# Kernel optimization log

Measured on AMD Instinct MI355X. Metric: run time of the kernel, lower is better.

The kernel has to match this reference:

```python
import jax, jax.numpy as jnp
import numpy as np

EMBED_DIM = 1024
ZDIM = 128
STD = 0.02


def setup_inputs() -> dict:
    key = jax.random.key(0)
    ks = jax.random.split(key, 12)
    T, S, B, E, Z = 2048, 2048, 4, EMBED_DIM, ZDIM
    return {
        "query": jax.random.normal(ks[0], (T, B, E), jnp.float32),
        "key": jax.random.normal(ks[1], (S, B, E), jnp.float32),
        "Wq": jax.random.normal(ks[2], (2 * E + Z, E), jnp.float32) * STD,
        "bq": jnp.zeros((2 * E + Z,), jnp.float32),
        "Wk": jax.random.normal(ks[3], (Z, E), jnp.float32) * STD,
        "bk": jnp.zeros((Z,), jnp.float32),
        "Wv": jax.random.normal(ks[4], (E, E), jnp.float32) * STD,
        "bv": jnp.zeros((E,), jnp.float32),
        "Wh": jax.random.normal(ks[5], (E, E), jnp.float32) * STD,
        "bh": jnp.zeros((E,), jnp.float32),
        "gamma": jax.random.normal(ks[6], (2, Z), jnp.float32) * STD,
        "beta": jnp.zeros((2, Z), jnp.float32),
    }


def reference(query, key, Wq, bq, Wk, bk, Wv, bv, Wh, bh, gamma, beta):
    E, Z = EMBED_DIM, ZDIM
    scaling = Z ** (-0.5)
    # base: [T, B, 2E+Z]
    base = jnp.einsum('tbe,fe->tbf', query, Wq) + bq
    u = jax.nn.sigmoid(base[..., :E])                      # [T,B,E] output gate
    rq = jax.nn.silu(base[..., E:])                        # [T,B,E+Z]
    r = rq[..., :E]                                        # [T,B,E]
    q = rq[..., E:] * gamma[0] + beta[0]                   # [T,B,Z]
    k = jax.nn.silu(jnp.einsum('sbe,ze->sbz', key, Wk) + bk) * gamma[1] + beta[1]  # [S,B,Z]
    v = jax.nn.silu(jnp.einsum('sbe,fe->sbf', key, Wv) + bv)                       # [S,B,E]
    # softmax attention over context dim
    qk = jnp.einsum('tbz,sbz->bts', q * scaling, k)        # [B,T,S]
    attn = jax.nn.softmax(qk, axis=-1)
    h = jnp.einsum('bts,sbf->tbf', attn, v)                # [T,B,E]
    h = jnp.tanh(jnp.einsum('tbe,fe->tbf', h * r, Wh) + bh)
    out = query + u * (h - query)                          # addcmul
    return out
```

## Files before the change

kernel.cpp:

```cpp
#include <hip/hip_runtime.h>
#include <cstdint>
#include <cstddef>

using short8  = __attribute__((ext_vector_type(8))) short;
using floatx4 = __attribute__((ext_vector_type(4))) float;

#define DEV __device__ __forceinline__

DEV float u2f(unsigned short u){
  union { unsigned int i; float f; } c; c.i = ((unsigned int)u) << 16; return c.f;
}
DEV unsigned short f2u(float f){
  union { float f; unsigned int i; } c; c.f = f;
  unsigned int i = c.i;
  i += 0x7fffu + ((i >> 16) & 1u);
  return (unsigned short)(i >> 16);
}
DEV float sigmoidf_(float x){ return 1.0f / (1.0f + __expf(-x)); }
DEV float siluf_(float x){ return x / (1.0f + __expf(-x)); }

#define ASYNC_LD16(g, l) __builtin_amdgcn_global_load_lds( \
    (const __attribute__((address_space(1))) unsigned int*)(g), \
    (__attribute__((address_space(3))) unsigned int*)(l), 16, 0, 0)

#define MFMA_BF16 __builtin_amdgcn_mfma_f32_16x16x32_bf16

#define SBAR() asm volatile("s_barrier" ::: "memory")
#define LGKM0() asm volatile("s_waitcnt lgkmcnt(0)" ::: "memory")

constexpr float SCALING = 0.088388347648318447f;

__global__ __launch_bounds__(256) void cast_all(
    const float* __restrict__ q, const float* __restrict__ k,
    const float* __restrict__ Wq, const float* __restrict__ Wk,
    const float* __restrict__ Wv, const float* __restrict__ Wh,
    unsigned short* __restrict__ qo, unsigned short* __restrict__ ko,
    unsigned short* __restrict__ oq, unsigned short* __restrict__ ok,
    unsigned short* __restrict__ ov, unsigned short* __restrict__ oh)
{
  const int bid = blockIdx.x;
  const int e = threadIdx.x * 4;
  const float* src; unsigned short* dst;
  if (bid < 8192) {
    src = q + (long long)bid * 1024;
    dst = qo + (long long)bid * 1024;
  } else if (bid < 16384) {
    const int m = bid - 8192;
    const int s = m >> 2, b = m & 3;
    src = k + (long long)m * 1024;
    dst = ko + ((long long)b * 2048 + s) * 1024;
  } else if (bid < 18560) { src = Wq + (long long)(bid-16384) * 1024; dst = oq + (long long)(bid-16384) * 1024; }
  else if (bid < 18688)   { src = Wk + (long long)(bid-18560) * 1024; dst = ok + (long long)(bid-18560) * 1024; }
  else if (bid < 19712)   { src = Wv + (long long)(bid-18688) * 1024; dst = ov + (long long)(bid-18688) * 1024; }
  else                    { src = Wh + (long long)(bid-19712) * 1024; dst = oh + (long long)(bid-19712) * 1024; }
  const float4 v = *(const float4*)(src + e);
  ushort4 o; o.x=f2u(v.x); o.y=f2u(v.y); o.z=f2u(v.z); o.w=f2u(v.w);
  *(ushort4*)(dst + e) = o;
}

__global__ __launch_bounds__(512, 2)
void mega(const unsigned short* __restrict__ qbf,
          const unsigned short* __restrict__ Wqb,
          const unsigned short* __restrict__ kbr,
          const unsigned short* __restrict__ Wvb,
          const unsigned short* __restrict__ Wkb,
          const float* __restrict__ bq, const float* __restrict__ bk,
          const float* __restrict__ bv,
          const float* __restrict__ gamma, const float* __restrict__ beta,
          float* __restrict__ ub_f,
          unsigned short* __restrict__ rbf,
          unsigned short* __restrict__ vT,
          unsigned short* __restrict__ qpj,
          unsigned short* __restrict__ kpj)
{
  __shared__ __align__(16) unsigned short Ls[65536];

  const int bid = blockIdx.x;
  const int tid = threadIdx.x;
  const int lane = tid & 63;
  const int wv   = tid >> 6;
  const int lr   = lane & 15;
  const int lq   = lane >> 4;
  const int r7   = lr & 7;

  const floatx4 zero = {0.f, 0.f, 0.f, 0.f};

  if (bid < 256) {
    const int bm = bid & 31, bn = bid >> 5;
    const int row0 = bm * 256;
    const int col0 = bn * 256;
    const int lda = 1024, ldb = 1024;
    const int wr = (wv >> 2) * 128;
    const int wc = (wv & 3) * 64;

    const int rr0 = tid >> 3;
    const int swz = ((tid & 7) ^ (rr0 & 7)) * 8;
    const unsigned short* gA0 = qbf + (long long)(row0 + rr0) * lda + swz;
    const unsigned short* gB0 = Wqb + (long long)(col0 + rr0) * ldb + swz;
    const long long sA64 = 64LL * lda, sB64 = 64LL * ldb;
    unsigned short* lA0 = &Ls[0]     + tid * 8;
    unsigned short* lB0 = &Ls[16384] + tid * 8;

    floatx4 acc[8][4];
    #pragma unroll
    for (int i = 0; i < 8; i++)
      #pragma unroll
      for (int j = 0; j < 4; j++) acc[i][j] = zero;

    const int NT = 16;

    #pragma unroll
    for (int i = 0; i < 4; i++) ASYNC_LD16(gA0 + i * sA64,      lA0 + i * 4096);
    #pragma unroll
    for (int i = 0; i < 4; i++) ASYNC_LD16(gB0 + i * sB64,      lB0 + i * 4096);
    #pragma unroll
    for (int i = 0; i < 4; i++) ASYNC_LD16(gA0 + i * sA64 + 64, lA0 + i * 4096 + 32768);
    #pragma unroll
    for (int i = 0; i < 4; i++) ASYNC_LD16(gB0 + i * sB64 + 64, lB0 + i * 4096 + 32768);
    asm volatile("s_waitcnt vmcnt(8)" ::: "memory");
    SBAR();

    for (int t = 0; t < NT; ++t) {
      const int cb = (t & 1) << 15;
      const unsigned short* Ab = &Ls[cb];
      const unsigned short* Bb = &Ls[cb + 16384];
      const bool st = (t + 2) < NT;
      const int kt2 = (t + 2) << 6;

      short8 afA[4][2], afB[4][2], bf01[2][2], bf23[2][2];

      #pragma unroll
      for (int mi = 0; mi < 4; mi++)
        #pragma unroll
        for (int kk = 0; kk < 2; kk++)
          afA[mi][kk] = *(const short8*)(Ab + (wr + mi*16 + lr) * 64 + (((kk<<2) + lq) ^ r7) * 8);
      #pragma unroll
      for (int ni = 0; ni < 2; ni++)
        #pragma unroll
        for (int kk = 0; kk < 2; kk++)
          bf01[ni][kk] = *(const short8*)(Bb + (wc + ni*16 + lr) * 64 + (((kk<<2) + lq) ^ r7) * 8);
      #pragma unroll
      for (int ni = 0; ni < 2; ni++)
        #pragma unroll
        for (int kk = 0; kk < 2; kk++)
          bf23[ni][kk] = *(const short8*)(Bb + (wc + (ni+2)*16 + lr) * 64 + (((kk<<2) + lq) ^ r7) * 8);
      __builtin_amdgcn_s_setprio(1);
      #pragma unroll
      for (int mi = 0; mi < 4; mi++)
        #pragma unroll
        for (int ni = 0; ni < 2; ni++)
          #pragma unroll
          for (int kk = 0; kk < 2; kk++)
            acc[mi][ni] = MFMA_BF16(afA[mi][kk], bf01[ni][kk], acc[mi][ni], 0, 0, 0);
      #pragma unroll
      for (int mi = 0; mi < 4; mi++)
        #pragma unroll
        for (int ni = 0; ni < 2; ni++)
          #pragma unroll
          for (int kk = 0; kk < 2; kk++)
            acc[mi][ni+2] = MFMA_BF16(afA[mi][kk], bf23[ni][kk], acc[mi][ni+2], 0, 0, 0);
      __builtin_amdgcn_s_setprio(0);
      LGKM0();
      SBAR();

      #pragma unroll
      for (int mi = 0; mi < 4; mi++)
        #pragma unroll
        for (int kk = 0; kk < 2; kk++)
          afB[mi][kk] = *(const short8*)(Ab + (wr + (mi+4)*16 + lr) * 64 + (((kk<<2) + lq) ^ r7) * 8);
      if (st) {
        #pragma unroll
        for (int i = 0; i < 4; i++) ASYNC_LD16(gB0 + i * sB64 + kt2, lB0 + i * 4096 + cb);
      }
      __builtin_amdgcn_s_setprio(1);
      #pragma unroll
      for (int mi = 0; mi < 4; mi++)
        #pragma unroll
        for (int ni = 0; ni < 2; ni++)
          #pragma unroll
          for (int kk = 0; kk < 2; kk++)
            acc[mi+4][ni] = MFMA_BF16(afB[mi][kk], bf01[ni][kk], acc[mi+4][ni], 0, 0, 0);
      __builtin_amdgcn_s_setprio(0);
      LGKM0();
      SBAR();

      if (st) {
        #pragma unroll
        for (int i = 0; i < 4; i++) ASYNC_LD16(gA0 + i * sA64 + kt2, lA0 + i * 4096 + cb);
      }
      __builtin_amdgcn_s_setprio(1);
      #pragma unroll
      for (int mi = 0; mi < 4; mi++)
        #pragma unroll
        for (int ni = 0; ni < 2; ni++)
          #pragma unroll
          for (int kk = 0; kk < 2; kk++)
            acc[mi+4][ni+2] = MFMA_BF16(afB[mi][kk], bf23[ni][kk], acc[mi+4][ni+2], 0, 0, 0);
      __builtin_amdgcn_s_setprio(0);
      if (st) { asm volatile("s_waitcnt vmcnt(8)" ::: "memory"); }
      else    { asm volatile("s_waitcnt vmcnt(0)" ::: "memory"); }
      SBAR();
    }

    #pragma unroll
    for (int mi = 0; mi < 8; mi++)
      #pragma unroll
      for (int ni = 0; ni < 4; ni++)
        #pragma unroll
        for (int r = 0; r < 4; r++) {
          const int gm = row0 + wr + mi * 16 + lq * 4 + r;
          const int gn = col0 + wc + ni * 16 + lr;
          float v = acc[mi][ni][r] + bq[gn];
          if (gn < 1024) {
            ((unsigned short*)ub_f)[(long long)gm * 1024 + gn] = f2u(sigmoidf_(v));
          } else {
            rbf[(long long)gm * 1024 + (gn - 1024)] = f2u(siluf_(v));
          }
        }
  } else {
    const unsigned short* Ag; const unsigned short* Bg;
    int row0, col0, zproj = -1;
    if (bid < 512) {
      const int idx = bid - 256;
      row0 = (idx & 3) * 256;
      col0 = (idx >> 2) * 128;
      Ag = Wvb; Bg = kbr;
    } else {
      const int idx = bid - 512;
      zproj = idx >> 5;
      row0 = (idx & 31) * 256;
      col0 = 0;
      Ag = zproj ? kbr : qbf;
      Bg = zproj ? Wkb : (Wqb + 2048LL * 1024);
    }
    const int lda = 1024, ldb = 1024;
    const int wr = (wv & 3) * 64;
    const int wc = (wv >> 2) * 64;

    const int rr0 = tid >> 3;
    const int swz = ((tid & 7) ^ (rr0 & 7)) * 8;
    const unsigned short* gA0 = Ag + (long long)(row0 + rr0) * lda + swz;
    const unsigned short* gB0 = Bg + (long long)(col0 + rr0) * ldb + swz;
    const long long sA64 = 64LL * lda, sB64 = 64LL * ldb;
    unsigned short* lA0 = &Ls[0]     + tid * 8;
    unsigned short* lB0 = &Ls[16384] + tid * 8;

    floatx4 acc[4][4];
    #pragma unroll
    for (int i = 0; i < 4; i++)
      #pragma unroll
      for (int j = 0; j < 4; j++) acc[i][j] = zero;

    const int NT = 16;

    #pragma unroll
    for (int i = 0; i < 4; i++) ASYNC_LD16(gA0 + i * sA64,      lA0 + i * 4096);
    #pragma unroll
    for (int i = 0; i < 2; i++) ASYNC_LD16(gB0 + i * sB64,      lB0 + i * 4096);
    #pragma unroll
    for (int i = 0; i < 4; i++) ASYNC_LD16(gA0 + i * sA64 + 64, lA0 + i * 4096 + 24576);
    #pragma unroll
    for (int i = 0; i < 2; i++) ASYNC_LD16(gB0 + i * sB64 + 64, lB0 + i * 4096 + 24576);
    asm volatile("s_waitcnt vmcnt(6)" ::: "memory");
    SBAR();

    for (int t = 0; t < NT; ++t) {
      const int cb = (t & 1) * 24576;
      const unsigned short* Ab = &Ls[cb];
      const unsigned short* Bb = &Ls[cb + 16384];
      const bool st = (t + 2) < NT;
      const int kt2 = (t + 2) << 6;

      short8 afA[4][2], bfv[4][2];

      #pragma unroll
      for (int mi = 0; mi < 4; mi++)
        #pragma unroll
        for (int kk = 0; kk < 2; kk++)
          afA[mi][kk] = *(const short8*)(Ab + (wr + mi*16 + lr) * 64 + (((kk<<2) + lq) ^ r7) * 8);
      #pragma unroll
      for (int ni = 0; ni < 4; ni++)
        #pragma unroll
        for (int kk = 0; kk < 2; kk++)
          bfv[ni][kk] = *(const short8*)(Bb + (wc + ni*16 + lr) * 64 + (((kk<<2) + lq) ^ r7) * 8);
      LGKM0();
      __builtin_amdgcn_sched_barrier(0);
      __builtin_amdgcn_s_setprio(1);
      #pragma unroll
      for (int mi = 0; mi < 4; mi++)
        #pragma unroll
        for (int ni = 0; ni < 2; ni++)
          #pragma unroll
          for (int kk = 0; kk < 2; kk++)
            acc[mi][ni] = MFMA_BF16(afA[mi][kk], bfv[ni][kk], acc[mi][ni], 0, 0, 0);
      __builtin_amdgcn_s_setprio(0);
      SBAR();

      if (st) {
        #pragma unroll
        for (int i = 0; i < 4; i++) ASYNC_LD16(gA0 + i * sA64 + kt2, lA0 + i * 4096 + cb);
        #pragma unroll
        for (int i = 0; i < 2; i++) ASYNC_LD16(gB0 + i * sB64 + kt2, lB0 + i * 4096 + cb);
      }
      __builtin_amdgcn_s_setprio(1);
      #pragma unroll
      for (int mi = 0; mi < 4; mi++)
        #pragma unroll
        for (int ni = 0; ni < 2; ni++)
          #pragma unroll
          for (int kk = 0; kk < 2; kk++)
            acc[mi][ni+2] = MFMA_BF16(afA[mi][kk], bfv[ni+2][kk], acc[mi][ni+2], 0, 0, 0);
      __builtin_amdgcn_s_setprio(0);
      if (st) { asm volatile("s_waitcnt vmcnt(6)" ::: "memory"); }
      else    { asm volatile("s_waitcnt vmcnt(0)" ::: "memory"); }
      SBAR();
    }

    if (zproj < 0) {
      #pragma unroll
      for (int mi = 0; mi < 4; mi++)
        #pragma unroll
        for (int ni = 0; ni < 4; ni++)
          #pragma unroll
          for (int r = 0; r < 4; r++) {
            const int gm = row0 + wr + mi * 16 + lq * 4 + r;
            const int gn = col0 + wc + ni * 16 + lr;
            const float v = acc[mi][ni][r] + bv[gm];
            const int b = gn >> 11, s = gn & 2047;
            vT[((long long)b * 1024 + gm) * 2048 + s] = f2u(siluf_(v));
          }
    } else {
      const float* bias = zproj ? bk : (bq + 2048);
      const float* gam  = zproj ? (gamma + 128) : gamma;
      const float* bet  = zproj ? (beta + 128)  : beta;
      unsigned short* ob = zproj ? kpj : qpj;
      #pragma unroll
      for (int mi = 0; mi < 4; mi++)
        #pragma unroll
        for (int ni = 0; ni < 4; ni++)
          #pragma unroll
          for (int r = 0; r < 4; r++) {
            const int gm = row0 + wr + mi * 16 + lq * 4 + r;
            const int gn = wc + ni * 16 + lr;
            const float v = acc[mi][ni][r] + bias[gn];
            ob[(long long)gm * 128 + gn] = f2u(siluf_(v) * gam[gn] + bet[gn]);
          }
    }
  }
}

__global__ __launch_bounds__(512, 2)
void gemm_g5(const unsigned short* __restrict__ A, int lda,
             const unsigned short* __restrict__ Bm, int ldb,
             int K,
             const float* __restrict__ bias,
             float* __restrict__ f0,
             const unsigned short* __restrict__ rmul,
             const float* __restrict__ qin)
{
  __shared__ __align__(16) unsigned short Ls[49152];

  const int tid = threadIdx.x;
  const int bm = blockIdx.x, bn = blockIdx.y;
  const int row0 = bm * 256;
  const int col0 = bn * 128;

  const int lane = tid & 63;
  const int wv   = tid >> 6;
  const int wr   = (wv & 3) * 64;
  const int wc   = (wv >> 2) * 64;
  const int lr   = lane & 15;
  const int lq   = lane >> 4;
  const int r7   = lr & 7;

  const int rr0 = tid >> 3;
  const int swz = ((tid & 7) ^ (rr0 & 7)) * 8;
  const unsigned short* gA0 = A  + (long long)(row0 + rr0) * lda + swz;
  const unsigned short* gB0 = Bm + (long long)(col0 + rr0) * ldb + swz;
  const long long sA64 = 64LL * lda, sB64 = 64LL * ldb;
  unsigned short* lA0 = &Ls[0]     + tid * 8;
  unsigned short* lB0 = &Ls[16384] + tid * 8;

  floatx4 acc[4][4];
  const floatx4 zero = {0.f, 0.f, 0.f, 0.f};
  #pragma unroll
  for (int i = 0; i < 4; i++)
    #pragma unroll
    for (int j = 0; j < 4; j++) acc[i][j] = zero;

  const int NT = K >> 6;

  #pragma unroll
  for (int i = 0; i < 4; i++) ASYNC_LD16(gA0 + i * sA64,      lA0 + i * 4096);
  #pragma unroll
  for (int i = 0; i < 2; i++) ASYNC_LD16(gB0 + i * sB64,      lB0 + i * 4096);
  #pragma unroll
  for (int i = 0; i < 4; i++) ASYNC_LD16(gA0 + i * sA64 + 64, lA0 + i * 4096 + 24576);
  #pragma unroll
  for (int i = 0; i < 2; i++) ASYNC_LD16(gB0 + i * sB64 + 64, lB0 + i * 4096 + 24576);
  asm volatile("s_waitcnt vmcnt(6)" ::: "memory");
  SBAR();

  for (int t = 0; t < NT; ++t) {
    const int cb = (t & 1) * 24576;
    const unsigned short* Ab = &Ls[cb];
    const unsigned short* Bb = &Ls[cb + 16384];
    const bool st = (t + 2) < NT;
    const int kt2 = (t + 2) << 6;

    short8 afA[4][2], bfv[4][2];

    #pragma unroll
    for (int mi = 0; mi < 4; mi++)
      #pragma unroll
      for (int kk = 0; kk < 2; kk++)
        afA[mi][kk] = *(const short8*)(Ab + (wr + mi*16 + lr) * 64 + (((kk<<2) + lq) ^ r7) * 8);
    #pragma unroll
    for (int ni = 0; ni < 4; ni++)
      #pragma unroll
      for (int kk = 0; kk < 2; kk++)
        bfv[ni][kk] = *(const short8*)(Bb + (wc + ni*16 + lr) * 64 + (((kk<<2) + lq) ^ r7) * 8);
    LGKM0();
    __builtin_amdgcn_sched_barrier(0);
    __builtin_amdgcn_s_setprio(1);
    #pragma unroll
    for (int mi = 0; mi < 4; mi++)
      #pragma unroll
      for (int ni = 0; ni < 2; ni++)
        #pragma unroll
        for (int kk = 0; kk < 2; kk++)
          acc[mi][ni] = MFMA_BF16(afA[mi][kk], bfv[ni][kk], acc[mi][ni], 0, 0, 0);
    __builtin_amdgcn_s_setprio(0);
    SBAR();

    if (st) {
      #pragma unroll
      for (int i = 0; i < 4; i++) ASYNC_LD16(gA0 + i * sA64 + kt2, lA0 + i * 4096 + cb);
      #pragma unroll
      for (int i = 0; i < 2; i++) ASYNC_LD16(gB0 + i * sB64 + kt2, lB0 + i * 4096 + cb);
    }
    __builtin_amdgcn_s_setprio(1);
    #pragma unroll
    for (int mi = 0; mi < 4; mi++)
      #pragma unroll
      for (int ni = 0; ni < 2; ni++)
        #pragma unroll
        for (int kk = 0; kk < 2; kk++)
          acc[mi][ni+2] = MFMA_BF16(afA[mi][kk], bfv[ni+2][kk], acc[mi][ni+2], 0, 0, 0);
    __builtin_amdgcn_s_setprio(0);
    if (st) { asm volatile("s_waitcnt vmcnt(6)" ::: "memory"); }
    else    { asm volatile("s_waitcnt vmcnt(0)" ::: "memory"); }
    SBAR();
  }

  #pragma unroll
  for (int mi = 0; mi < 4; mi++)
    #pragma unroll
    for (int ni = 0; ni < 4; ni++)
      #pragma unroll
      for (int r = 0; r < 4; r++) {
        const int gm = row0 + wr + mi * 16 + lq * 4 + r;
        const int gn = col0 + wc + ni * 16 + lr;
        const long long idx = (long long)gm * 1024 + gn;
        const float tv = tanhf(acc[mi][ni][r] + bias[gn]);
        const float qv = qin[idx];
        f0[idx] = qv + u2f(rmul[idx]) * (tv - qv);
      }
}

__global__ __launch_bounds__(512, 2)
void attn_fused(const unsigned short* __restrict__ qpj,
                const unsigned short* __restrict__ kpj,
                const unsigned short* __restrict__ vT,
                const unsigned short* __restrict__ rbf,
                unsigned short* __restrict__ hrb)
{
  __shared__ __align__(16) unsigned short Vs[32768];
  __shared__ __align__(16) unsigned short Ks[2][8192];
  __shared__ __align__(16) unsigned short Ps[4096];
  __shared__ float rsl[64];

  const int tid = threadIdx.x;
  const int eh = blockIdx.x, ty = blockIdx.y, bz = blockIdx.z;
  const int t0 = ty * 64;

  const int lane = tid & 63;
  const int wv   = tid >> 6;
  const int lr   = lane & 15;
  const int lq   = lane >> 4;
  const int mi_s = wv & 3;
  const int niA  = (wv >> 2) * 2;

  const unsigned short* kb_g = kpj + (long long)bz * 2048 * 128;
  const unsigned short* vb_g = vT  + (long long)bz * 1024 * 2048;

  short8 afq[4];
  {
    const unsigned short* qrow = qpj + (long long)bz * 128
                               + (long long)(t0 + mi_s * 16 + lr) * 512;
    #pragma unroll
    for (int kd = 0; kd < 4; kd++)
      afq[kd] = *(const short8*)(qrow + (kd * 4 + lq) * 8);
  }

  const int rrV = tid >> 3;
  const int gcV = ((tid & 7) ^ (rrV & 7)) * 8;
  const unsigned short* gV0 = vb_g + (long long)(eh * 512 + rrV) * 2048 + gcV;
  unsigned short* lV0 = Vs + tid * 8;
  const int rrK = tid >> 4;
  const int gcK = ((tid & 15) ^ (rrK & 15)) * 8;
  const unsigned short* gK0 = kb_g + (long long)rrK * 128 + gcK;
  unsigned short* lK0 = &Ks[0][0] + tid * 8;

  floatx4 acc[4][4];
  floatx4 accSum[4];
  const floatx4 zero = {0.f, 0.f, 0.f, 0.f};
  #pragma unroll
  for (int i = 0; i < 4; i++) {
    accSum[i] = zero;
    #pragma unroll
    for (int j = 0; j < 4; j++) acc[i][j] = zero;
  }
  const short ob = (short)0x3F80;
  const short8 ones = {ob, ob, ob, ob, ob, ob, ob, ob};

  #pragma unroll
  for (int i = 0; i < 2; i++) ASYNC_LD16(gK0 + i * 4096, lK0 + i * 4096);

  for (int t = 0; t < 32; ++t) {
    const unsigned short* Kb = &Ks[t & 1][0];
    const bool st = (t + 1) < 32;

    #pragma unroll
    for (int i = 0; i < 8; i++)
      ASYNC_LD16(gV0 + (long long)i * 131072 + t * 64, lV0 + i * 4096);
    if (st) {
      unsigned short* lKn = &Ks[(t + 1) & 1][0] + tid * 8;
      #pragma unroll
      for (int i = 0; i < 2; i++)
        ASYNC_LD16(gK0 + (long long)(t + 1) * 8192 + i * 4096, lKn + i * 4096);
    }
    if (st) { asm volatile("s_waitcnt vmcnt(10)" ::: "memory"); }
    else    { asm volatile("s_waitcnt vmcnt(8)"  ::: "memory"); }
    SBAR();

    floatx4 accS[2] = {zero, zero};
    short8 bfk[2][4];
    #pragma unroll
    for (int f = 0; f < 2; f++)
      #pragma unroll
      for (int kd = 0; kd < 4; kd++)
        bfk[f][kd] = *(const short8*)(Kb + ((niA + f) * 16 + lr) * 128
                                         + (((kd * 4 + lq) ^ lr) & 15) * 8);
    #pragma unroll
    for (int f = 0; f < 2; f++)
      #pragma unroll
      for (int kd = 0; kd < 4; kd++)
        accS[f] = MFMA_BF16(afq[kd], bfk[f][kd], accS[f], 0, 0, 0);
    #pragma unroll
    for (int f = 0; f < 2; f++) {
      const int nif = niA + f;
      #pragma unroll
      for (int r = 0; r < 4; r++) {
        const float e = __expf(accS[f][r] * SCALING);
        const int trow = mi_s * 16 + lq * 4 + r;
        const int scol = nif * 16 + lr;
        const int slot = (scol >> 3) ^ (trow & 7);
        Ps[trow * 64 + slot * 8 + (lr & 7)] = f2u(e);
      }
    }
    LGKM0();
    if (st) { asm volatile("s_waitcnt vmcnt(2)" ::: "memory"); }
    else    { asm volatile("s_waitcnt vmcnt(0)" ::: "memory"); }
    SBAR();

    short8 afP[4][2], bfv[4][2];
    #pragma unroll
    for (int mi = 0; mi < 4; mi++)
      #pragma unroll
      for (int k8 = 0; k8 < 2; k8++)
        afP[mi][k8] = *(const short8*)(Ps + (mi * 16 + lr) * 64
                                          + ((k8 * 4 + lq) ^ (lr & 7)) * 8);
    #pragma unroll
    for (int ni = 0; ni < 4; ni++)
      #pragma unroll
      for (int k8 = 0; k8 < 2; k8++)
        bfv[ni][k8] = *(const short8*)(Vs + (wv * 64 + ni * 16 + lr) * 64
                                          + ((k8 * 4 + lq) ^ (lr & 7)) * 8);
    __builtin_amdgcn_s_setprio(1);
    #pragma unroll
    for (int mi = 0; mi < 4; mi++)
      #pragma unroll
      for (int ni = 0; ni < 4; ni++)
        #pragma unroll
        for (int k8 = 0; k8 < 2; k8++)
          acc[mi][ni] = MFMA_BF16(afP[mi][k8], bfv[ni][k8], acc[mi][ni], 0, 0, 0);
    __builtin_amdgcn_s_setprio(0);
    if (wv == 0) {
      #pragma unroll
      for (int mi = 0; mi < 4; mi++)
        #pragma unroll
        for (int k8 = 0; k8 < 2; k8++)
          accSum[mi] = MFMA_BF16(afP[mi][k8], ones, accSum[mi], 0, 0, 0);
    }
    LGKM0();
    SBAR();
  }

  if (wv == 0 && lr == 0) {
    #pragma unroll
    for (int mi = 0; mi < 4; mi++)
      #pragma unroll
      for (int r = 0; r < 4; r++)
        rsl[mi * 16 + lq * 4 + r] = accSum[mi][r];
  }
  LGKM0();
  SBAR();
  #pragma unroll
  for (int mi = 0; mi < 4; mi++) {
    float iv[4];
    #pragma unroll
    for (int r = 0; r < 4; r++) iv[r] = 1.0f / rsl[mi * 16 + lq * 4 + r];
    #pragma unroll
    for (int ni = 0; ni < 4; ni++) {
      #pragma unroll
      for (int r = 0; r < 4; r++) {
        const int gt = t0 + mi * 16 + lq * 4 + r;
        const int ge = eh * 512 + wv * 64 + ni * 16 + lr;
        const long long idx = ((long long)gt * 4 + bz) * 1024 + ge;
        hrb[idx] = f2u(acc[mi][ni][r] * iv[r] * u2f(rbf[idx]));
      }
    }
  }
}

extern "C" void kernel_launch(void* const* d_in, const int* in_sizes, int n_in,
                              void* d_out, int out_size, void* d_ws, size_t ws_size,
                              hipStream_t stream)
{
  (void)in_sizes; (void)n_in; (void)out_size; (void)ws_size;
  const float* query = (const float*)d_in[0];
  const float* key   = (const float*)d_in[1];
  const float* Wq    = (const float*)d_in[2];
  const float* bq    = (const float*)d_in[3];
  const float* Wk    = (const float*)d_in[4];
  const float* bk    = (const float*)d_in[5];
  const float* Wv    = (const float*)d_in[6];
  const float* bv    = (const float*)d_in[7];
  const float* Wh    = (const float*)d_in[8];
  const float* bh    = (const float*)d_in[9];
  const float* gamma = (const float*)d_in[10];
  const float* beta  = (const float*)d_in[11];
  float* out = (float*)d_out;

  char* p = (char*)d_ws;
  auto take = [&](size_t bytes) -> char* {
    char* r = p; p += (bytes + 255) & ~(size_t)255; return r;
  };
  unsigned short* qbf = (unsigned short*)take(8192ULL * 1024 * 2);
  unsigned short* kbr = (unsigned short*)take(8192ULL * 1024 * 2);
  unsigned short* Wqb = (unsigned short*)take(2176ULL * 1024 * 2);
  unsigned short* Wkb = (unsigned short*)take(128ULL  * 1024 * 2);
  unsigned short* Wvb = (unsigned short*)take(1024ULL * 1024 * 2);
  unsigned short* Whb = (unsigned short*)take(1024ULL * 1024 * 2);
  unsigned short* ub  = (unsigned short*)take(8192ULL * 1024 * 2);
  unsigned short* rbf = (unsigned short*)take(8192ULL * 1024 * 2);
  unsigned short* qpj = (unsigned short*)take(8192ULL * 128 * 2);
  unsigned short* kpj = (unsigned short*)take(8192ULL * 128 * 2);
  unsigned short* vT  = (unsigned short*)take(4ULL * 1024 * 2048 * 2);
  unsigned short* hrb = (unsigned short*)take(8192ULL * 1024 * 2);

  dim3 blk(256);
  dim3 gblk(512);
  cast_all<<<20736, blk, 0, stream>>>(query, key, Wq, Wk, Wv, Wh,
      qbf, kbr, Wqb, Wkb, Wvb, Whb);
  mega<<<576, gblk, 0, stream>>>(qbf, Wqb, kbr, Wvb, Wkb,
      bq, bk, bv, gamma, beta, (float*)ub, rbf, vT, qpj, kpj);
  attn_fused<<<dim3(2, 32, 4), gblk, 0, stream>>>(qpj, kpj, vT, rbf, hrb);
  gemm_g5<<<dim3(32, 8, 1), gblk, 0, stream>>>(hrb, 1024, Whb, 1024, 1024,
      bh, out, ub, query);
}
```

Measured before the change: 330.7 us.

## Fuse all stages into one cooperative persistent kernel with grid syncs

```diff
diff --git a/kernel.cpp b/kernel.cpp
--- a/kernel.cpp
+++ b/kernel.cpp
@@ -1,6 +1,9 @@
 #include <hip/hip_runtime.h>
+#include <hip/hip_cooperative_groups.h>
 #include <cstdint>
 #include <cstddef>
+
+namespace cg = cooperative_groups;
 
 using short8  = __attribute__((ext_vector_type(8))) short;
 using floatx4 = __attribute__((ext_vector_type(4))) float;
@@ -30,63 +33,44 @@
 
 constexpr float SCALING = 0.088388347648318447f;
 
-__global__ __launch_bounds__(256) void cast_all(
-    const float* __restrict__ q, const float* __restrict__ k,
-    const float* __restrict__ Wq, const float* __restrict__ Wk,
-    const float* __restrict__ Wv, const float* __restrict__ Wh,
-    unsigned short* __restrict__ qo, unsigned short* __restrict__ ko,
-    unsigned short* __restrict__ oq, unsigned short* __restrict__ ok,
-    unsigned short* __restrict__ ov, unsigned short* __restrict__ oh)
-{
-  const int bid = blockIdx.x;
-  const int e = threadIdx.x * 4;
+struct KP {
+  const float *query, *key, *Wq, *bq, *Wk, *bk, *Wv, *bv, *Wh, *bh, *gamma, *beta;
+  float* out;
+  unsigned short *qbf, *kbr, *Wqb, *Wkb, *Wvb, *Whb, *ub, *rbf, *qpj, *kpj, *vT, *hrb;
+  int* wq;
+};
+
+DEV void dev_cast(int r, int e, const KP& p)
+{
   const float* src; unsigned short* dst;
-  if (bid < 8192) {
-    src = q + (long long)bid * 1024;
-    dst = qo + (long long)bid * 1024;
-  } else if (bid < 16384) {
-    const int m = bid - 8192;
+  if (r < 8192) {
+    src = p.query + (long long)r * 1024;
+    dst = p.qbf   + (long long)r * 1024;
+  } else if (r < 16384) {
+    const int m = r - 8192;
     const int s = m >> 2, b = m & 3;
-    src = k + (long long)m * 1024;
-    dst = ko + ((long long)b * 2048 + s) * 1024;
-  } else if (bid < 18560) { src = Wq + (long long)(bid-16384) * 1024; dst = oq + (long long)(bid-16384) * 1024; }
-  else if (bid < 18688)   { src = Wk + (long long)(bid-18560) * 1024; dst = ok + (long long)(bid-18560) * 1024; }
-  else if (bid < 19712)   { src = Wv + (long long)(bid-18688) * 1024; dst = ov + (long long)(bid-18688) * 1024; }
-  else                    { src = Wh + (long long)(bid-19712) * 1024; dst = oh + (long long)(bid-19712) * 1024; }
+    src = p.key + (long long)m * 1024;
+    dst = p.kbr + ((long long)b * 2048 + s) * 1024;
+  } else if (r < 18560) { src = p.Wq + (long long)(r-16384) * 1024; dst = p.Wqb + (long long)(r-16384) * 1024; }
+  else if (r < 18688)   { src = p.Wk + (long long)(r-18560) * 1024; dst = p.Wkb + (long long)(r-18560) * 1024; }
+  else if (r < 19712)   { src = p.Wv + (long long)(r-18688) * 1024; dst = p.Wvb + (long long)(r-18688) * 1024; }
+  else                  { src = p.Wh + (long long)(r-19712) * 1024; dst = p.Whb + (long long)(r-19712) * 1024; }
   const float4 v = *(const float4*)(src + e);
   ushort4 o; o.x=f2u(v.x); o.y=f2u(v.y); o.z=f2u(v.z); o.w=f2u(v.w);
   *(ushort4*)(dst + e) = o;
 }
 
-__global__ __launch_bounds__(512, 2)
-void mega(const unsigned short* __restrict__ qbf,
-          const unsigned short* __restrict__ Wqb,
-          const unsigned short* __restrict__ kbr,
-          const unsigned short* __restrict__ Wvb,
-          const unsigned short* __restrict__ Wkb,
-          const float* __restrict__ bq, const float* __restrict__ bk,
-          const float* __restrict__ bv,
-          const float* __restrict__ gamma, const float* __restrict__ beta,
-          float* __restrict__ ub_f,
-          unsigned short* __restrict__ rbf,
-          unsigned short* __restrict__ vT,
-          unsigned short* __restrict__ qpj,
-          unsigned short* __restrict__ kpj)
-{
-  __shared__ __align__(16) unsigned short Ls[65536];
-
-  const int bid = blockIdx.x;
-  const int tid = threadIdx.x;
+DEV void dev_mega(int lb, unsigned short* __restrict__ Ls, const KP& p, int tid)
+{
   const int lane = tid & 63;
   const int wv   = tid >> 6;
   const int lr   = lane & 15;
   const int lq   = lane >> 4;
   const int r7   = lr & 7;
-
   const floatx4 zero = {0.f, 0.f, 0.f, 0.f};
 
-  if (bid < 256) {
-    const int bm = bid & 31, bn = bid >> 5;
+  if (lb < 256) {
+    const int bm = lb & 31, bn = lb >> 5;
     const int row0 = bm * 256;
     const int col0 = bn * 256;
     const int lda = 1024, ldb = 1024;
@@ -95,11 +79,11 @@
 
     const int rr0 = tid >> 3;
     const int swz = ((tid & 7) ^ (rr0 & 7)) * 8;
-    const unsigned short* gA0 = qbf + (long long)(row0 + rr0) * lda + swz;
-    const unsigned short* gB0 = Wqb + (long long)(col0 + rr0) * ldb + swz;
+    const unsigned short* gA0 = p.qbf + (long long)(row0 + rr0) * lda + swz;
+    const unsigned short* gB0 = p.Wqb + (long long)(col0 + rr0) * ldb + swz;
     const long long sA64 = 64LL * lda, sB64 = 64LL * ldb;
-    unsigned short* lA0 = &Ls[0]     + tid * 8;
-    unsigned short* lB0 = &Ls[16384] + tid * 8;
+    unsigned short* lA0 = Ls         + tid * 8;
+    unsigned short* lB0 = Ls + 16384 + tid * 8;
 
     floatx4 acc[8][4];
     #pragma unroll
@@ -122,8 +106,8 @@
 
     for (int t = 0; t < NT; ++t) {
       const int cb = (t & 1) << 15;
-      const unsigned short* Ab = &Ls[cb];
-      const unsigned short* Bb = &Ls[cb + 16384];
+      const unsigned short* Ab = Ls + cb;
+      const unsigned short* Bb = Ls + cb + 16384;
       const bool st = (t + 2) < NT;
       const int kt2 = (t + 2) << 6;
 
@@ -210,28 +194,28 @@
         for (int r = 0; r < 4; r++) {
           const int gm = row0 + wr + mi * 16 + lq * 4 + r;
           const int gn = col0 + wc + ni * 16 + lr;
-          float v = acc[mi][ni][r] + bq[gn];
+          float v = acc[mi][ni][r] + p.bq[gn];
           if (gn < 1024) {
-            ((unsigned short*)ub_f)[(long long)gm * 1024 + gn] = f2u(sigmoidf_(v));
+            p.ub[(long long)gm * 1024 + gn] = f2u(sigmoidf_(v));
           } else {
-            rbf[(long long)gm * 1024 + (gn - 1024)] = f2u(siluf_(v));
+            p.rbf[(long long)gm * 1024 + (gn - 1024)] = f2u(siluf_(v));
           }
         }
   } else {
     const unsigned short* Ag; const unsigned short* Bg;
     int row0, col0, zproj = -1;
-    if (bid < 512) {
-      const int idx = bid - 256;
+    if (lb < 512) {
+      const int idx = lb - 256;
       row0 = (idx & 3) * 256;
       col0 = (idx >> 2) * 128;
-      Ag = Wvb; Bg = kbr;
+      Ag = p.Wvb; Bg = p.kbr;
     } else {
-      const int idx = bid - 512;
+      const int idx = lb - 512;
       zproj = idx >> 5;
       row0 = (idx & 31) * 256;
       col0 = 0;
-      Ag = zproj ? kbr : qbf;
-      Bg = zproj ? Wkb : (Wqb + 2048LL * 1024);
+      Ag = zproj ? p.kbr : p.qbf;
+      Bg = zproj ? p.Wkb : (p.Wqb + 2048LL * 1024);
     }
     const int lda = 1024, ldb = 1024;
     const int wr = (wv & 3) * 64;
@@ -242,8 +226,8 @@
     const unsigned short* gA0 = Ag + (long long)(row0 + rr0) * lda + swz;
     const unsigned short* gB0 = Bg + (long long)(col0 + rr0) * ldb + swz;
     const long long sA64 = 64LL * lda, sB64 = 64LL * ldb;
-    unsigned short* lA0 = &Ls[0]     + tid * 8;
-    unsigned short* lB0 = &Ls[16384] + tid * 8;
+    unsigned short* lA0 = Ls         + tid * 8;
+    unsigned short* lB0 = Ls + 16384 + tid * 8;
 
     floatx4 acc[4][4];
     #pragma unroll
@@ -266,8 +250,8 @@
 
     for (int t = 0; t < NT; ++t) {
       const int cb = (t & 1) * 24576;
-      const unsigned short* Ab = &Ls[cb];
-      const unsigned short* Bb = &Ls[cb + 16384];
+      const unsigned short* Ab = Ls + cb;
+      const unsigned short* Bb = Ls + cb + 16384;
       const bool st = (t + 2) < NT;
       const int kt2 = (t + 2) << 6;
 
@@ -325,15 +309,15 @@
           for (int r = 0; r < 4; r++) {
             const int gm = row0 + wr + mi * 16 + lq * 4 + r;
             const int gn = col0 + wc + ni * 16 + lr;
-            const float v = acc[mi][ni][r] + bv[gm];
+            const float v = acc[mi][ni][r] + p.bv[gm];
             const int b = gn >> 11, s = gn & 2047;
-            vT[((long long)b * 1024 + gm) * 2048 + s] = f2u(siluf_(v));
+            p.vT[((long long)b * 1024 + gm) * 2048 + s] = f2u(siluf_(v));
           }
     } else {
-      const float* bias = zproj ? bk : (bq + 2048);
-      const float* gam  = zproj ? (gamma + 128) : gamma;
-      const float* bet  = zproj ? (beta + 128)  : beta;
-      unsigned short* ob = zproj ? kpj : qpj;
+      const float* bias = zproj ? p.bk : (p.bq + 2048);
+      const float* gam  = zproj ? (p.gamma + 128) : p.gamma;
+      const float* bet  = zproj ? (p.beta + 128)  : p.beta;
+      unsigned short* ob = zproj ? p.kpj : p.qpj;
       #pragma unroll
       for (int mi = 0; mi < 4; mi++)
         #pragma unroll
@@ -349,21 +333,172 @@
   }
 }
 
-__global__ __launch_bounds__(512, 2)
-void gemm_g5(const unsigned short* __restrict__ A, int lda,
-             const unsigned short* __restrict__ Bm, int ldb,
-             int K,
-             const float* __restrict__ bias,
-             float* __restrict__ f0,
-             const unsigned short* __restrict__ rmul,
-             const float* __restrict__ qin)
-{
-  __shared__ __align__(16) unsigned short Ls[49152];
-
-  const int tid = threadIdx.x;
-  const int bm = blockIdx.x, bn = blockIdx.y;
+DEV void dev_attn(int bid, unsigned char* __restrict__ pool, const KP& p, int tid)
+{
+  unsigned short* Vs = (unsigned short*)(pool);
+  unsigned short* Ks = (unsigned short*)(pool + 65536);
+  unsigned short* Ps = (unsigned short*)(pool + 98304);
+  float*         rsl = (float*)(pool + 106496);
+
+  const int eh = bid & 1, ty = (bid >> 1) & 31, bz = bid >> 6;
+  const int t0 = ty * 64;
+
+  const int lane = tid & 63;
+  const int wv   = tid >> 6;
+  const int lr   = lane & 15;
+  const int lq   = lane >> 4;
+  const int mi_s = wv & 3;
+  const int niA  = (wv >> 2) * 2;
+
+  const unsigned short* kb_g = p.kpj + (long long)bz * 2048 * 128;
+  const unsigned short* vb_g = p.vT  + (long long)bz * 1024 * 2048;
+
+  short8 afq[4];
+  {
+    const unsigned short* qrow = p.qpj + (long long)bz * 128
+                               + (long long)(t0 + mi_s * 16 + lr) * 512;
+    #pragma unroll
+    for (int kd = 0; kd < 4; kd++)
+      afq[kd] = *(const short8*)(qrow + (kd * 4 + lq) * 8);
+  }
+
+  const int rrV = tid >> 3;
+  const int gcV = ((tid & 7) ^ (rrV & 7)) * 8;
+  const unsigned short* gV0 = vb_g + (long long)(eh * 512 + rrV) * 2048 + gcV;
+  unsigned short* lV0 = Vs + tid * 8;
+  const int rrK = tid >> 4;
+  const int gcK = ((tid & 15) ^ (rrK & 15)) * 8;
+  const unsigned short* gK0 = kb_g + (long long)rrK * 128 + gcK;
+  unsigned short* lK0 = Ks + tid * 8;
+
+  floatx4 acc[4][4];
+  floatx4 accSum[4];
+  const floatx4 zero = {0.f, 0.f, 0.f, 0.f};
+  #pragma unroll
+  for (int i = 0; i < 4; i++) {
+    accSum[i] = zero;
+    #pragma unroll
+    for (int j = 0; j < 4; j++) acc[i][j] = zero;
+  }
+  const short ob = (short)0x3F80;
+  const short8 ones = {ob, ob, ob, ob, ob, ob, ob, ob};
+
+  #pragma unroll
+  for (int i = 0; i < 2; i++) ASYNC_LD16(gK0 + i * 4096, lK0 + i * 4096);
+
+  for (int t = 0; t < 32; ++t) {
+    const unsigned short* Kb = Ks + (t & 1) * 8192;
+    const bool st = (t + 1) < 32;
+
+    #pragma unroll
+    for (int i = 0; i < 8; i++)
+      ASYNC_LD16(gV0 + (long long)i * 131072 + t * 64, lV0 + i * 4096);
+    if (st) {
+      unsigned short* lKn = Ks + ((t + 1) & 1) * 8192 + tid * 8;
+      #pragma unroll
+      for (int i = 0; i < 2; i++)
+        ASYNC_LD16(gK0 + (long long)(t + 1) * 8192 + i * 4096, lKn + i * 4096);
+    }
+    if (st) { asm volatile("s_waitcnt vmcnt(10)" ::: "memory"); }
+    else    { asm volatile("s_waitcnt vmcnt(8)"  ::: "memory"); }
+    SBAR();
+
+    floatx4 accS[2] = {zero, zero};
+    short8 bfk[2][4];
+    #pragma unroll
+    for (int f = 0; f < 2; f++)
+      #pragma unroll
+      for (int kd = 0; kd < 4; kd++)
+        bfk[f][kd] = *(const short8*)(Kb + ((niA + f) * 16 + lr) * 128
+                                         + (((kd * 4 + lq) ^ lr) & 15) * 8);
+    #pragma unroll
+    for (int f = 0; f < 2; f++)
+      #pragma unroll
+      for (int kd = 0; kd < 4; kd++)
+        accS[f] = MFMA_BF16(afq[kd], bfk[f][kd], accS[f], 0, 0, 0);
+    #pragma unroll
+    for (int f = 0; f < 2; f++) {
+      const int nif = niA + f;
+      #pragma unroll
+      for (int r = 0; r < 4; r++) {
+        const float e = __expf(accS[f][r] * SCALING);
+        const int trow = mi_s * 16 + lq * 4 + r;
+        const int scol = nif * 16 + lr;
+        const int slot = (scol >> 3) ^ (trow & 7);
+        Ps[trow * 64 + slot * 8 + (lr & 7)] = f2u(e);
+      }
+    }
+    LGKM0();
+    if (st) { asm volatile("s_waitcnt vmcnt(2)" ::: "memory"); }
+    else    { asm volatile("s_waitcnt vmcnt(0)" ::: "memory"); }
+    SBAR();
+
+    short8 afP[4][2], bfv[4][2];
+    #pragma unroll
+    for (int mi = 0; mi < 4; mi++)
+      #pragma unroll
+      for (int k8 = 0; k8 < 2; k8++)
+        afP[mi][k8] = *(const short8*)(Ps + (mi * 16 + lr) * 64
+                                          + ((k8 * 4 + lq) ^ (lr & 7)) * 8);
+    #pragma unroll
+    for (int ni = 0; ni < 4; ni++)
+      #pragma unroll
+      for (int k8 = 0; k8 < 2; k8++)
+        bfv[ni][k8] = *(const short8*)(Vs + (wv * 64 + ni * 16 + lr) * 64
+                                          + ((k8 * 4 + lq) ^ (lr & 7)) * 8);
+    __builtin_amdgcn_s_setprio(1);
+    #pragma unroll
+    for (int mi = 0; mi < 4; mi++)
+      #pragma unroll
+      for (int ni = 0; ni < 4; ni++)
+        #pragma unroll
+        for (int k8 = 0; k8 < 2; k8++)
+          acc[mi][ni] = MFMA_BF16(afP[mi][k8], bfv[ni][k8], acc[mi][ni], 0, 0, 0);
+    __builtin_amdgcn_s_setprio(0);
+    if (wv == 0) {
+      #pragma unroll
+      for (int mi = 0; mi < 4; mi++)
+        #pragma unroll
+        for (int k8 = 0; k8 < 2; k8++)
+          accSum[mi] = MFMA_BF16(afP[mi][k8], ones, accSum[mi], 0, 0, 0);
+    }
+    LGKM0();
+    SBAR();
+  }
+
+  if (wv == 0 && lr == 0) {
+    #pragma unroll
+    for (int mi = 0; mi < 4; mi++)
+      #pragma unroll
+      for (int r = 0; r < 4; r++)
+        rsl[mi * 16 + lq * 4 + r] = accSum[mi][r];
+  }
+  LGKM0();
+  SBAR();
+  #pragma unroll
+  for (int mi = 0; mi < 4; mi++) {
+    float iv[4];
+    #pragma unroll
+    for (int r = 0; r < 4; r++) iv[r] = 1.0f / rsl[mi * 16 + lq * 4 + r];
+    #pragma unroll
+    for (int ni = 0; ni < 4; ni++) {
+      #pragma unroll
+      for (int r = 0; r < 4; r++) {
+        const int gt = t0 + mi * 16 + lq * 4 + r;
+        const int ge = eh * 512 + wv * 64 + ni * 16 + lr;
+        const long long idx = ((long long)gt * 4 + bz) * 1024 + ge;
+        p.hrb[idx] = f2u(acc[mi][ni][r] * iv[r] * u2f(p.rbf[idx]));
+      }
+    }
+  }
+}
+
+DEV void dev_g5(int bid, unsigned short* __restrict__ Ls, const KP& p, int tid)
+{
+  const int bm = bid & 31, bn = bid >> 5;
   const int row0 = bm * 256;
   const int col0 = bn * 128;
+  const int lda = 1024, ldb = 1024;
 
   const int lane = tid & 63;
   const int wv   = tid >> 6;
@@ -375,11 +510,11 @@
 
   const int rr0 = tid >> 3;
   const int swz = ((tid & 7) ^ (rr0 & 7)) * 8;
-  const unsigned short* gA0 = A  + (long long)(row0 + rr0) * lda + swz;
-  const unsigned short* gB0 = Bm + (long long)(col0 + rr0) * ldb + swz;
+  const unsigned short* gA0 = p.hrb + (long long)(row0 + rr0) * lda + swz;
+  const unsigned short* gB0 = p.Whb + (long long)(col0 + rr0) * ldb + swz;
   const long long sA64 = 64LL * lda, sB64 = 64LL * ldb;
-  unsigned short* lA0 = &Ls[0]     + tid * 8;
-  unsigned short* lB0 = &Ls[16384] + tid * 8;
+  unsigned short* lA0 = Ls         + tid * 8;
+  unsigned short* lB0 = Ls + 16384 + tid * 8;
 
   floatx4 acc[4][4];
   const floatx4 zero = {0.f, 0.f, 0.f, 0.f};
@@ -388,7 +523,7 @@
     #pragma unroll
     for (int j = 0; j < 4; j++) acc[i][j] = zero;
 
-  const int NT = K >> 6;
+  const int NT = 16;
 
   #pragma unroll
   for (int i = 0; i < 4; i++) ASYNC_LD16(gA0 + i * sA64,      lA0 + i * 4096);
@@ -403,8 +538,8 @@
 
   for (int t = 0; t < NT; ++t) {
     const int cb = (t & 1) * 24576;
-    const unsigned short* Ab = &Ls[cb];
-    const unsigned short* Bb = &Ls[cb + 16384];
+    const unsigned short* Ab = Ls + cb;
+    const unsigned short* Bb = Ls + cb + 16384;
     const bool st = (t + 2) < NT;
     const int kt2 = (t + 2) << 6;
 
@@ -462,176 +597,64 @@
         const int gm = row0 + wr + mi * 16 + lq * 4 + r;
         const int gn = col0 + wc + ni * 16 + lr;
         const long long idx = (long long)gm * 1024 + gn;
-        const float tv = tanhf(acc[mi][ni][r] + bias[gn]);
-        const float qv = qin[idx];
-        f0[idx] = qv + u2f(rmul[idx]) * (tv - qv);
+        const float tv = tanhf(acc[mi][ni][r] + p.bh[gn]);
+        const float qv = p.query[idx];
+        p.out[idx] = qv + u2f(p.ub[idx]) * (tv - qv);
       }
 }
 
-__global__ __launch_bounds__(512, 2)
-void attn_fused(const unsigned short* __restrict__ qpj,
-                const unsigned short* __restrict__ kpj,
-                const unsigned short* __restrict__ vT,
-                const unsigned short* __restrict__ rbf,
-                unsigned short* __restrict__ hrb)
-{
-  __shared__ __align__(16) unsigned short Vs[32768];
-  __shared__ __align__(16) unsigned short Ks[2][8192];
-  __shared__ __align__(16) unsigned short Ps[4096];
-  __shared__ float rsl[64];
-
+__global__ __launch_bounds__(512, 2) void uber(KP p)
+{
+  __shared__ __align__(16) unsigned char pool[131072];
+  __shared__ int lb_sh;
   const int tid = threadIdx.x;
-  const int eh = blockIdx.x, ty = blockIdx.y, bz = blockIdx.z;
-  const int t0 = ty * 64;
-
-  const int lane = tid & 63;
-  const int wv   = tid >> 6;
-  const int lr   = lane & 15;
-  const int lq   = lane >> 4;
-  const int mi_s = wv & 3;
-  const int niA  = (wv >> 2) * 2;
-
-  const unsigned short* kb_g = kpj + (long long)bz * 2048 * 128;
-  const unsigned short* vb_g = vT  + (long long)bz * 1024 * 2048;
-
-  short8 afq[4];
-  {
-    const unsigned short* qrow = qpj + (long long)bz * 128
-                               + (long long)(t0 + mi_s * 16 + lr) * 512;
-    #pragma unroll
-    for (int kd = 0; kd < 4; kd++)
-      afq[kd] = *(const short8*)(qrow + (kd * 4 + lq) * 8);
-  }
-
-  const int rrV = tid >> 3;
-  const int gcV = ((tid & 7) ^ (rrV & 7)) * 8;
-  const unsigned short* gV0 = vb_g + (long long)(eh * 512 + rrV) * 2048 + gcV;
-  unsigned short* lV0 = Vs + tid * 8;
-  const int rrK = tid >> 4;
-  const int gcK = ((tid & 15) ^ (rrK & 15)) * 8;
-  const unsigned short* gK0 = kb_g + (long long)rrK * 128 + gcK;
-  unsigned short* lK0 = &Ks[0][0] + tid * 8;
-
-  floatx4 acc[4][4];
-  floatx4 accSum[4];
-  const floatx4 zero = {0.f, 0.f, 0.f, 0.f};
-  #pragma unroll
-  for (int i = 0; i < 4; i++) {
-    accSum[i] = zero;
-    #pragma unroll
-    for (int j = 0; j < 4; j++) acc[i][j] = zero;
-  }
-  const short ob = (short)0x3F80;
-  const short8 ones = {ob, ob, ob, ob, ob, ob, ob, ob};
-
-  #pragma unroll
-  for (int i = 0; i < 2; i++) ASYNC_LD16(gK0 + i * 4096, lK0 + i * 4096);
-
-  for (int t = 0; t < 32; ++t) {
-    const unsigned short* Kb = &Ks[t & 1][0];
-    const bool st = (t + 1) < 32;
-
-    #pragma unroll
-    for (int i = 0; i < 8; i++)
-      ASYNC_LD16(gV0 + (long long)i * 131072 + t * 64, lV0 + i * 4096);
-    if (st) {
-      unsigned short* lKn = &Ks[(t + 1) & 1][0] + tid * 8;
-      #pragma unroll
-      for (int i = 0; i < 2; i++)
-        ASYNC_LD16(gK0 + (long long)(t + 1) * 8192 + i * 4096, lKn + i * 4096);
-    }
-    if (st) { asm volatile("s_waitcnt vmcnt(10)" ::: "memory"); }
-    else    { asm volatile("s_waitcnt vmcnt(8)"  ::: "memory"); }
-    SBAR();
-
-    floatx4 accS[2] = {zero, zero};
-    short8 bfk[2][4];
-    #pragma unroll
-    for (int f = 0; f < 2; f++)
-      #pragma unroll
-      for (int kd = 0; kd < 4; kd++)
-        bfk[f][kd] = *(const short8*)(Kb + ((niA + f) * 16 + lr) * 128
-                                         + (((kd * 4 + lq) ^ lr) & 15) * 8);
-    #pragma unroll
-    for (int f = 0; f < 2; f++)
-      #pragma unroll
-      for (int kd = 0; kd < 4; kd++)
-        accS[f] = MFMA_BF16(afq[kd], bfk[f][kd], accS[f], 0, 0, 0);
-    #pragma unroll
-    for (int f = 0; f < 2; f++) {
-      const int nif = niA + f;
-      #pragma unroll
-      for (int r = 0; r < 4; r++) {
-        const float e = __expf(accS[f][r] * SCALING);
-        const int trow = mi_s * 16 + lq * 4 + r;
-        const int scol = nif * 16 + lr;
-        const int slot = (scol >> 3) ^ (trow & 7);
-        Ps[trow * 64 + slot * 8 + (lr & 7)] = f2u(e);
-      }
-    }
-    LGKM0();
-    if (st) { asm volatile("s_waitcnt vmcnt(2)" ::: "memory"); }
-    else    { asm volatile("s_waitcnt vmcnt(0)" ::: "memory"); }
-    SBAR();
-
-    short8 afP[4][2], bfv[4][2];
-    #pragma unroll
-    for (int mi = 0; mi < 4; mi++)
-      #pragma unroll
-      for (int k8 = 0; k8 < 2; k8++)
-        afP[mi][k8] = *(const short8*)(Ps + (mi * 16 + lr) * 64
-                                          + ((k8 * 4 + lq) ^ (lr & 7)) * 8);
-    #pragma unroll
-    for (int ni = 0; ni < 4; ni++)
-      #pragma unroll
-      for (int k8 = 0; k8 < 2; k8++)
-        bfv[ni][k8] = *(const short8*)(Vs + (wv * 64 + ni * 16 + lr) * 64
-                                          + ((k8 * 4 + lq) ^ (lr & 7)) * 8);
-    __builtin_amdgcn_s_setprio(1);
-    #pragma unroll
-    for (int mi = 0; mi < 4; mi++)
-      #pragma unroll
-      for (int ni = 0; ni < 4; ni++)
-        #pragma unroll
-        for (int k8 = 0; k8 < 2; k8++)
-          acc[mi][ni] = MFMA_BF16(afP[mi][k8], bfv[ni][k8], acc[mi][ni], 0, 0, 0);
-    __builtin_amdgcn_s_setprio(0);
-    if (wv == 0) {
-      #pragma unroll
-      for (int mi = 0; mi < 4; mi++)
-        #pragma unroll
-        for (int k8 = 0; k8 < 2; k8++)
-          accSum[mi] = MFMA_BF16(afP[mi][k8], ones, accSum[mi], 0, 0, 0);
-    }
-    LGKM0();
-    SBAR();
-  }
-
-  if (wv == 0 && lr == 0) {
-    #pragma unroll
-    for (int mi = 0; mi < 4; mi++)
-      #pragma unroll
-      for (int r = 0; r < 4; r++)
-        rsl[mi * 16 + lq * 4 + r] = accSum[mi][r];
-  }
-  LGKM0();
-  SBAR();
-  #pragma unroll
-  for (int mi = 0; mi < 4; mi++) {
-    float iv[4];
-    #pragma unroll
-    for (int r = 0; r < 4; r++) iv[r] = 1.0f / rsl[mi * 16 + lq * 4 + r];
-    #pragma unroll
-    for (int ni = 0; ni < 4; ni++) {
-      #pragma unroll
-      for (int r = 0; r < 4; r++) {
-        const int gt = t0 + mi * 16 + lq * 4 + r;
-        const int ge = eh * 512 + wv * 64 + ni * 16 + lr;
-        const long long idx = ((long long)gt * 4 + bz) * 1024 + ge;
-        hrb[idx] = f2u(acc[mi][ni][r] * iv[r] * u2f(rbf[idx]));
-      }
-    }
-  }
+  const int bid = blockIdx.x;
+  cg::grid_group grid = cg::this_grid();
+
+  for (int pp = bid; pp < 10368; pp += 256) {
+    dev_cast(pp * 2 + (tid >> 8), (tid & 255) * 4, p);
+  }
+  if (bid == 0 && tid == 0) *p.wq = 0;
+  __threadfence();
+  grid.sync();
+
+  unsigned short* Ls = (unsigned short*)pool;
+  for (;;) {
+    if (tid == 0) lb_sh = atomicAdd(p.wq, 1);
+    __syncthreads();
+    const int lb = lb_sh;
+    if (lb >= 576) break;
+    dev_mega(lb, Ls, p, tid);
+    __syncthreads();
+  }
+  __threadfence();
+  grid.sync();
+
+  dev_attn(bid, pool, p, tid);
+  __threadfence();
+  grid.sync();
+
+  dev_g5(bid, Ls, p, tid);
+}
+
+__global__ __launch_bounds__(256) void k_cast(KP p)
+{
+  dev_cast(blockIdx.x, threadIdx.x * 4, p);
+}
+__global__ __launch_bounds__(512, 2) void k_mega(KP p)
+{
+  __shared__ __align__(16) unsigned short Ls[65536];
+  dev_mega(blockIdx.x, Ls, p, threadIdx.x);
+}
+__global__ __launch_bounds__(512, 2) void k_attn(KP p)
+{
+  __shared__ __align__(16) unsigned char pool[106752];
+  dev_attn(blockIdx.x, pool, p, threadIdx.x);
+}
+__global__ __launch_bounds__(512, 2) void k_g5(KP p)
+{
+  __shared__ __align__(16) unsigned short Ls[49152];
+  dev_g5(blockIdx.x, Ls, p, threadIdx.x);
 }
 
 extern "C" void kernel_launch(void* const* d_in, const int* in_sizes, int n_in,
@@ -639,44 +662,47 @@
                               hipStream_t stream)
 {
   (void)in_sizes; (void)n_in; (void)out_size; (void)ws_size;
-  const float* query = (const float*)d_in[0];
-  const float* key   = (const float*)d_in[1];
-  const float* Wq    = (const float*)d_in[2];
-  const float* bq    = (const float*)d_in[3];
-  const float* Wk    = (const float*)d_in[4];
-  const float* bk    = (const float*)d_in[5];
-  const float* Wv    = (const float*)d_in[6];
-  const float* bv    = (const float*)d_in[7];
-  const float* Wh    = (const float*)d_in[8];
-  const float* bh    = (const float*)d_in[9];
-  const float* gamma = (const float*)d_in[10];
-  const float* beta  = (const float*)d_in[11];
-  float* out = (float*)d_out;
-
-  char* p = (char*)d_ws;
+
+  char* wp = (char*)d_ws;
   auto take = [&](size_t bytes) -> char* {
-    char* r = p; p += (bytes + 255) & ~(size_t)255; return r;
+    char* r = wp; wp += (bytes + 255) & ~(size_t)255; return r;
   };
-  unsigned short* qbf = (unsigned short*)take(8192ULL * 1024 * 2);
-  unsigned short* kbr = (unsigned short*)take(8192ULL * 1024 * 2);
-  unsigned short* Wqb = (unsigned short*)take(2176ULL * 1024 * 2);
-  unsigned short* Wkb = (unsigned short*)take(128ULL  * 1024 * 2);
-  unsigned short* Wvb = (unsigned short*)take(1024ULL * 1024 * 2);
-  unsigned short* Whb = (unsigned short*)take(1024ULL * 1024 * 2);
-  unsigned short* ub  = (unsigned short*)take(8192ULL * 1024 * 2);
-  unsigned short* rbf = (unsigned short*)take(8192ULL * 1024 * 2);
-  unsigned short* qpj = (unsigned short*)take(8192ULL * 128 * 2);
-  unsigned short* kpj = (unsigned short*)take(8192ULL * 128 * 2);
-  unsigned short* vT  = (unsigned short*)take(4ULL * 1024 * 2048 * 2);
-  unsigned short* hrb = (unsigned short*)take(8192ULL * 1024 * 2);
-
-  dim3 blk(256);
-  dim3 gblk(512);
-  cast_all<<<20736, blk, 0, stream>>>(query, key, Wq, Wk, Wv, Wh,
-      qbf, kbr, Wqb, Wkb, Wvb, Whb);
-  mega<<<576, gblk, 0, stream>>>(qbf, Wqb, kbr, Wvb, Wkb,
-      bq, bk, bv, gamma, beta, (float*)ub, rbf, vT, qpj, kpj);
-  attn_fused<<<dim3(2, 32, 4), gblk, 0, stream>>>(qpj, kpj, vT, rbf, hrb);
-  gemm_g5<<<dim3(32, 8, 1), gblk, 0, stream>>>(hrb, 1024, Whb, 1024, 1024,
-      bh, out, ub, query);
-}
+  KP p;
+  p.query = (const float*)d_in[0];
+  p.key   = (const float*)d_in[1];
+  p.Wq    = (const float*)d_in[2];
+  p.bq    = (const float*)d_in[3];
+  p.Wk    = (const float*)d_in[4];
+  p.bk    = (const float*)d_in[5];
+  p.Wv    = (const float*)d_in[6];
+  p.bv    = (const float*)d_in[7];
+  p.Wh    = (const float*)d_in[8];
+  p.bh    = (const float*)d_in[9];
+  p.gamma = (const float*)d_in[10];
+  p.beta  = (const float*)d_in[11];
+  p.out   = (float*)d_out;
+  p.qbf = (unsigned short*)take(8192ULL * 1024 * 2);
+  p.kbr = (unsigned short*)take(8192ULL * 1024 * 2);
+  p.Wqb = (unsigned short*)take(2176ULL * 1024 * 2);
+  p.Wkb = (unsigned short*)take(128ULL  * 1024 * 2);
+  p.Wvb = (unsigned short*)take(1024ULL * 1024 * 2);
+  p.Whb = (unsigned short*)take(1024ULL * 1024 * 2);
+  p.ub  = (unsigned short*)take(8192ULL * 1024 * 2);
+  p.rbf = (unsigned short*)take(8192ULL * 1024 * 2);
+  p.qpj = (unsigned short*)take(8192ULL * 128 * 2);
+  p.kpj = (unsigned short*)take(8192ULL * 128 * 2);
+  p.vT  = (unsigned short*)take(4ULL * 1024 * 2048 * 2);
+  p.hrb = (unsigned short*)take(8192ULL * 1024 * 2);
+  p.wq  = (int*)take(256);
+
+  void* args[] = { (void*)&p };
+  hipError_t err = hipLaunchCooperativeKernel((const void*)uber,
+                                              dim3(256), dim3(512),
+                                              args, 0, stream);
+  if (err != hipSuccess) {
+    k_cast<<<20736, 256, 0, stream>>>(p);
+    k_mega<<<576, 512, 0, stream>>>(p);
+    k_attn<<<256, 512, 0, stream>>>(p);
+    k_g5<<<256, 512, 0, stream>>>(p);
+  }
+}
```

Measured after the change: 624.0 us. 1.89x slower.
